# Optimization experiments

Measured on AMD Instinct MI355X. Metric: run time of the kernel, lower is better.

Reference implementation:

```python
import jax, jax.numpy as jnp
import numpy as np

DIM = 4096
N_HEADS = 32
N_KV_HEADS = 8
HEAD_DIM = DIM // N_HEADS  # 128
N_REP = N_HEADS // N_KV_HEADS  # 4
HIDDEN = 14336  # 4*dim -> 2/3 -> *1.3 -> round up to multiple of 256
EPS = 1e-6
BSZ, SEQLEN, CACHE_LEN = 1, 2048, 4096
ROPE_THETA = 500000.0


def setup_inputs() -> dict:
    key = jax.random.key(0)
    ks = jax.random.split(key, 16)
    s = 0.02
    x = jax.random.normal(ks[0], (BSZ, SEQLEN, DIM), jnp.float32)
    cache_k = jax.random.normal(ks[1], (BSZ, CACHE_LEN, N_KV_HEADS, HEAD_DIM), jnp.float32)
    cache_v = jax.random.normal(ks[2], (BSZ, CACHE_LEN, N_KV_HEADS, HEAD_DIM), jnp.float32)
    # causal mask over rolling cache: query i may attend to cache slot j <= (CACHE_LEN - SEQLEN) + i
    qi = jnp.arange(SEQLEN)[:, None]
    kj = jnp.arange(CACHE_LEN)[None, :]
    mask = jnp.where(kj <= (CACHE_LEN - SEQLEN) + qi, 0.0, -1e9).astype(jnp.float32)[None, None]
    # rotary freqs (cos/sin pairs) for the new seqlen positions (start of window here)
    inv = 1.0 / (ROPE_THETA ** (jnp.arange(0, HEAD_DIM, 2, dtype=jnp.float32) / HEAD_DIM))
    t = jnp.arange(SEQLEN, dtype=jnp.float32)
    ang = t[:, None] * inv[None, :]  # [S, HEAD_DIM//2]
    freqs_cis = jnp.stack([jnp.cos(ang), jnp.sin(ang)], axis=-1)  # [S, HD//2, 2]
    # params (stored as (in, out))
    wq = jax.random.normal(ks[3], (DIM, N_HEADS * HEAD_DIM), jnp.float32) * s
    wk = jax.random.normal(ks[4], (DIM, N_KV_HEADS * HEAD_DIM), jnp.float32) * s
    wv = jax.random.normal(ks[5], (DIM, N_KV_HEADS * HEAD_DIM), jnp.float32) * s
    wo = jax.random.normal(ks[6], (N_HEADS * HEAD_DIM, DIM), jnp.float32) * s
    w1 = jax.random.normal(ks[7], (DIM, HIDDEN), jnp.float32) * s
    w2 = jax.random.normal(ks[8], (HIDDEN, DIM), jnp.float32) * s
    w3 = jax.random.normal(ks[9], (DIM, HIDDEN), jnp.float32) * s
    attn_norm_w = jnp.ones((DIM,), jnp.float32)
    ffn_norm_w = jnp.ones((DIM,), jnp.float32)
    return dict(x=x, mask=mask, freqs_cis=freqs_cis, cache_k=cache_k, cache_v=cache_v,
                wq=wq, wk=wk, wv=wv, wo=wo, w1=w1, w2=w2, w3=w3,
                attn_norm_w=attn_norm_w, ffn_norm_w=ffn_norm_w)


def rmsnorm(x, w, eps=EPS):
    return x * jax.lax.rsqrt(jnp.mean(x * x, axis=-1, keepdims=True) + eps) * w


def apply_rope(xq, xk, freqs_cis):
    # xq: [B,S,Hq,D], xk: [B,S,Hkv,D]; freqs_cis: [S, D//2, 2]
    cos = freqs_cis[None, :, None, :, 0]  # [1,S,1,D//2]
    sin = freqs_cis[None, :, None, :, 1]
    def rot(t):
        tp = t.reshape(*t.shape[:-1], -1, 2)
        t0, t1 = tp[..., 0], tp[..., 1]
        o0 = t0 * cos - t1 * sin
        o1 = t0 * sin + t1 * cos
        return jnp.stack([o0, o1], axis=-1).reshape(t.shape)
    return rot(xq), rot(xk)


def reference(x, mask, freqs_cis, cache_k, cache_v, wq, wk, wv, wo, w1, w2, w3, attn_norm_w, ffn_norm_w):
    bsz, seqlen, _ = x.shape
    # --- attention norm ---
    xn = rmsnorm(x, attn_norm_w)
    # --- qkv ---
    xq = (xn @ wq).reshape(bsz, seqlen, N_HEADS, HEAD_DIM)
    xk = (xn @ wk).reshape(bsz, seqlen, N_KV_HEADS, HEAD_DIM)
    xv = (xn @ wv).reshape(bsz, seqlen, N_KV_HEADS, HEAD_DIM)
    xq, xk = apply_rope(xq, xk, freqs_cis)
    # --- rolling KV cache ---
    cache_k = jnp.concatenate([cache_k[:, seqlen:], xk], axis=1)  # [B,CL,Hkv,D]
    cache_v = jnp.concatenate([cache_v[:, seqlen:], xv], axis=1)
    keys = jnp.repeat(cache_k[:bsz], N_REP, axis=2)    # [B,CL,Hq,D]
    values = jnp.repeat(cache_v[:bsz], N_REP, axis=2)
    # --- attention ---
    scores = jnp.einsum('bqhd,bkhd->bhqk', xq, keys) / jnp.sqrt(jnp.float32(HEAD_DIM))
    scores = jax.nn.softmax(scores + mask, axis=-1)
    attn = jnp.einsum('bhqk,bkhd->bqhd', scores, values).reshape(bsz, seqlen, -1)
    h = x + attn @ wo
    # --- ffn (SwiGLU) ---
    hn = rmsnorm(h, ffn_norm_w)
    out = h + (jax.nn.silu(hn @ w1) * (hn @ w3)) @ w2
    return (out, cache_k, cache_v)
```

## Files before the change

kernel.cpp:

```cpp
#include <hip/hip_runtime.h>

typedef _Float16 h16;
typedef _Float16 h16x4 __attribute__((ext_vector_type(4)));
typedef _Float16 h16x8 __attribute__((ext_vector_type(8)));
typedef __fp16 fp16x2 __attribute__((ext_vector_type(2)));
typedef float f32x4 __attribute__((ext_vector_type(4)));
typedef float f32x16 __attribute__((ext_vector_type(16)));
typedef unsigned short u16;
typedef unsigned int u32;
typedef unsigned int u32x4 __attribute__((ext_vector_type(4)));

__device__ __forceinline__ f32x4 mfma16(h16x8 a, h16x8 b, f32x4 c) {
  return __builtin_amdgcn_mfma_f32_16x16x32_f16(a, b, c, 0, 0, 0);
}
__device__ __forceinline__ f32x16 mfma32(h16x8 a, h16x8 b, f32x16 c) {
  return __builtin_amdgcn_mfma_f32_32x32x16_f16(a, b, c, 0, 0, 0);
}
__device__ __forceinline__ float fexp2(float x) {
#if __has_builtin(__builtin_amdgcn_exp2f)
  return __builtin_amdgcn_exp2f(x);
#else
  return exp2f(x);
#endif
}
__device__ __forceinline__ u32 pkh(float a, float b) {
  fp16x2 t = __builtin_amdgcn_cvt_pkrtz(a, b);
  return __builtin_bit_cast(u32, t);
}

typedef const __attribute__((address_space(1))) void* gas_p;
typedef __attribute__((address_space(3))) void* las_p;
__device__ __forceinline__ void ldscp16(const void* g, void* l) {
  __builtin_amdgcn_global_load_lds((gas_p)g, (las_p)l, 16, 0, 0);
}
#define VMCNT(n) asm volatile("s_waitcnt vmcnt(" #n ")" ::: "memory")
#define SBAR() asm volatile("s_barrier" ::: "memory")

__global__ __launch_bounds__(256) void rmsnorm_k(
    const float* __restrict__ x, const float* __restrict__ w, h16* __restrict__ out) {
  const int row = blockIdx.x, t = threadIdx.x;
  const float* xr = x + (size_t)row * 4096;
  float4 v[4];
  float ss = 0.f;
#pragma unroll
  for (int j = 0; j < 4; j++) {
    v[j] = *(const float4*)(xr + 4 * t + 1024 * j);
    ss += v[j].x * v[j].x + v[j].y * v[j].y + v[j].z * v[j].z + v[j].w * v[j].w;
  }
#pragma unroll
  for (int off = 1; off < 64; off <<= 1) ss += __shfl_xor(ss, off, 64);
  __shared__ float red[4];
  if ((t & 63) == 0) red[t >> 6] = ss;
  __syncthreads();
  float scale = rsqrtf((red[0] + red[1] + red[2] + red[3]) * (1.f / 4096.f) + 1e-6f);
  h16* orow = out + (size_t)row * 4096;
#pragma unroll
  for (int j = 0; j < 4; j++) {
    float4 wv = *(const float4*)(w + 4 * t + 1024 * j);
    h16x4 o;
    o[0] = (h16)(v[j].x * scale * wv.x);
    o[1] = (h16)(v[j].y * scale * wv.y);
    o[2] = (h16)(v[j].z * scale * wv.z);
    o[3] = (h16)(v[j].w * scale * wv.w);
    *(h16x4*)(orow + 4 * t + 1024 * j) = o;
  }
}

__global__ __launch_bounds__(256) void convw_k(
    const float* __restrict__ W, h16* __restrict__ out, int rowN, int ktiles) {
  __shared__ u16 timg[8192];
  const int t = threadIdx.x, b = blockIdx.x, kt = blockIdx.y;
  const float* src = W + (size_t)(kt * 64) * rowN + b * 128;
#pragma unroll
  for (int i = 0; i < 8; i++) {
    int c = t + (i << 8);
    int krow = c >> 5, nc = (c & 31) << 2;
    float4 v = *(const float4*)(src + (size_t)krow * rowN + nc);
    int kc = krow >> 3, e = krow & 7;
    float vals[4] = {v.x, v.y, v.z, v.w};
#pragma unroll
    for (int j = 0; j < 4; j++) {
      int m = nc + j;
      h16 hv = (h16)vals[j];
      timg[(m << 6) + ((kc ^ (m & 7)) << 3) + e] = __builtin_bit_cast(u16, hv);
    }
  }
  __syncthreads();
  uint4* dst = (uint4*)(out + ((size_t)(b * ktiles + kt) << 13));
  const uint4* s4 = (const uint4*)timg;
#pragma unroll
  for (int i = 0; i < 4; i++) dst[t + (i << 8)] = s4[t + (i << 8)];
}

template <int EPI>
__global__ __launch_bounds__(512, 2) void gemm_k(
    const h16* __restrict__ A, const h16* __restrict__ Wt,
    float* outF, h16* outH, const float* resid, const h16* uin,
    int K, int lda, int ldo, int no0) {
  __shared__ u16 lds[3][24576];
  const int tid = threadIdx.x, lane = tid & 63;
  const int wv = tid >> 6, wr = wv >> 2, wc = wv & 3;
  const int g = lane >> 4, lr = lane & 15;
  const int m0 = blockIdx.y << 7, n0 = blockIdx.x << 8;
  const int ktiles = K >> 6;

  f32x4 acc[4][4];
#pragma unroll
  for (int i = 0; i < 4; i++)
#pragma unroll
    for (int j = 0; j < 4; j++) acc[i][j] = {0.f, 0.f, 0.f, 0.f};

  const int rA = tid >> 3;
  const int kcA = (tid & 7) ^ (rA & 7);
  const h16* gA = A + (size_t)(m0 + rA) * lda + (kcA << 3);
  const h16* gA2 = gA + (size_t)64 * lda;
  const h16* gB0 = Wt + (((size_t)(2 * blockIdx.x) * ktiles) << 13) + tid * 8;
  const h16* gB1 = Wt + (((size_t)(2 * blockIdx.x + 1) * ktiles) << 13) + tid * 8;

  auto issueA = [&](int t) {
    char* base = (char*)lds[t % 3];
    ldscp16(gA + t * 64, base + tid * 16);
    ldscp16(gA2 + t * 64, base + tid * 16 + 8192);
    ldscp16(gB0 + ((size_t)t << 13), base + 16384 + tid * 16);
    ldscp16(gB0 + ((size_t)t << 13) + 4096, base + 16384 + tid * 16 + 8192);
  };
  auto issueB = [&](int t) {
    char* base = (char*)lds[t % 3];
    ldscp16(gB1 + ((size_t)t << 13), base + 32768 + tid * 16);
    ldscp16(gB1 + ((size_t)t << 13) + 4096, base + 32768 + tid * 16 + 8192);
  };

  issueA(0); issueB(0); issueA(1); issueB(1);
  VMCNT(6);
  SBAR();

  for (int t = 0; t < ktiles; ++t) {
    const char* bp = (const char*)lds[t % 3];
    const bool more = (t + 2 < ktiles);
#pragma unroll
    for (int ks = 0; ks < 2; ++ks) {
      h16x8 av[4], bv[4];
      const int cc = (ks << 2) + g;
#pragma unroll
      for (int f = 0; f < 4; f++) {
        int row = (wr << 6) + (f << 4) + lr;
        av[f] = *(const h16x8*)(bp + row * 128 + ((cc ^ (row & 7)) << 4));
        int nr = (wc << 6) + (f << 4) + lr;
        bv[f] = *(const h16x8*)(bp + 16384 + nr * 128 + ((cc ^ (nr & 7)) << 4));
      }
      if (more) {
        if (ks == 0) issueA(t + 2);
        else issueB(t + 2);
      }
      __builtin_amdgcn_s_setprio(1);
#pragma unroll
      for (int fi = 0; fi < 4; fi++)
#pragma unroll
        for (int fj = 0; fj < 4; fj++)
          acc[fi][fj] = mfma16(av[fi], bv[fj], acc[fi][fj]);
      __builtin_amdgcn_s_setprio(0);
    }
    if (t + 1 < ktiles) {
      if (more) VMCNT(6);
      else VMCNT(0);
      SBAR();
    }
  }
#pragma unroll
  for (int fi = 0; fi < 4; fi++) {
    const int row = m0 + (wr << 6) + (fi << 4) + (g << 2);
#pragma unroll
    for (int fj = 0; fj < 4; fj++) {
      const int col = no0 + n0 + (wc << 6) + (fj << 4) + lr;
#pragma unroll
      for (int r = 0; r < 4; r++) {
        float vl = acc[fi][fj][r];
        if constexpr (EPI == 5) {
          if (col < 4096) outH[(size_t)(row + r) * 4096 + col] = (h16)vl;
          else outF[(size_t)(row + r) * 2048 + (col - 4096)] = vl;
        } else {
          size_t idx = (size_t)(row + r) * ldo + col;
          if constexpr (EPI == 1) outH[idx] = (h16)vl;
          else if constexpr (EPI == 2) outF[idx] = resid[idx] + vl;
          else if constexpr (EPI == 3) {
            float u = (float)uin[idx];
            outH[idx] = (h16)((u / (1.f + __expf(-u))) * vl);
          } else outF[idx] = outF[idx] + vl;
        }
      }
    }
  }
}

__global__ __launch_bounds__(256) void rope_q_k(
    const h16* __restrict__ qin, const float* __restrict__ freqs, h16* qout) {
  const int row = blockIdx.x, t = threadIdx.x;
  const float SCL = 0.12751743647239037f;
#pragma unroll
  for (int it = 0; it < 8; ++it) {
    int pid = t + 256 * it;
    int head = pid >> 6, pp = pid & 63;
    size_t idx = (size_t)row * 4096 + head * 128 + 2 * pp;
    float x0 = (float)qin[idx], x1 = (float)qin[idx + 1];
    float cs = freqs[row * 128 + 2 * pp], sn = freqs[row * 128 + 2 * pp + 1];
    qout[idx] = (h16)((x0 * cs - x1 * sn) * SCL);
    qout[idx + 1] = (h16)((x0 * sn + x1 * cs) * SCL);
  }
}

__global__ __launch_bounds__(256) void cache_build_k(
    const float* __restrict__ oldK, const float* __restrict__ oldV,
    const float* __restrict__ kvraw, const float* __restrict__ freqs,
    float* __restrict__ outK, float* __restrict__ outV,
    h16* __restrict__ Kf, h16* __restrict__ Vt) {
  const int rt = blockIdx.x, kvh = blockIdx.y;
  const int r0 = rt * 64, tid = threadIdx.x;
  __shared__ u16 vtile[64][128];
#pragma unroll
  for (int it = 0; it < 16; ++it) {
    int s = tid + 256 * it;
    int rr = s >> 6, pp = s & 63;
    int r = r0 + rr;
    float k0, k1, v0, v1;
    if (r < 2048) {
      const float* kp = oldK + (size_t)(r + 2048) * 1024 + kvh * 128 + 2 * pp;
      k0 = kp[0]; k1 = kp[1];
      const float* vp = oldV + (size_t)(r + 2048) * 1024 + kvh * 128 + 2 * pp;
      v0 = vp[0]; v1 = vp[1];
    } else {
      int tpos = r - 2048;
      const float* kp = kvraw + (size_t)tpos * 2048 + kvh * 128 + 2 * pp;
      float x0 = kp[0], x1 = kp[1];
      float cs = freqs[tpos * 128 + 2 * pp], sn = freqs[tpos * 128 + 2 * pp + 1];
      k0 = x0 * cs - x1 * sn;
      k1 = x0 * sn + x1 * cs;
      const float* vp = kvraw + (size_t)tpos * 2048 + 1024 + kvh * 128 + 2 * pp;
      v0 = vp[0]; v1 = vp[1];
    }
    size_t oidx = (size_t)r * 1024 + kvh * 128 + 2 * pp;
    outK[oidx] = k0; outK[oidx + 1] = k1;
    outV[oidx] = v0; outV[oidx + 1] = v1;
    size_t kfi = (size_t)kvh * 524288 + (size_t)r * 128 + 2 * pp;
    Kf[kfi] = (h16)k0; Kf[kfi + 1] = (h16)k1;
    h16 h0 = (h16)v0, h1 = (h16)v1;
    vtile[rr][2 * pp] = __builtin_bit_cast(u16, h0);
    vtile[rr][2 * pp + 1] = __builtin_bit_cast(u16, h1);
  }
  __syncthreads();
#pragma unroll
  for (int it = 0; it < 4; ++it) {
    int c = tid + 256 * it;
    int d = c >> 3, rg = c & 7;
    u16 tmp[8];
#pragma unroll
    for (int u = 0; u < 8; u++) tmp[u] = vtile[rg * 8 + u][d];
    *(uint4*)((u16*)Vt + (size_t)kvh * 524288 + (size_t)d * 4096 + r0 + rg * 8) =
        *(uint4*)tmp;
  }
}

__global__ __launch_bounds__(256, 2) void attn_k(
    const h16* __restrict__ Q, const h16* __restrict__ Kf,
    const h16* __restrict__ Vt, h16* __restrict__ O) {
  __shared__ u16 skv[2][16384];
  const int qt = 15 - blockIdx.x, h = blockIdx.y;
  const int q0 = qt << 7, kvh = h >> 2;
  const int tid = threadIdx.x, w = tid >> 6, lane = tid & 63;
  const int lq = lane & 31, lh = lane >> 5;
  const h16* Kb = Kf + (size_t)kvh * 524288;
  const h16* Vb = Vt + (size_t)kvh * 524288;
  const int qg = q0 + w * 32 + lq;

  h16x8 qv[8];
  {
    const h16* qp = Q + (size_t)qg * 4096 + h * 128 + (lh << 3);
#pragma unroll
    for (int c = 0; c < 8; c++) qv[c] = *(const h16x8*)(qp + c * 16);
  }
  h16x8 hone;
#pragma unroll
  for (int i = 0; i < 8; i++) hone[i] = (h16)1.0f;
  f32x16 oa[4], ol2;
#pragma unroll
  for (int d = 0; d < 4; d++)
#pragma unroll
    for (int v = 0; v < 16; v++) oa[d][v] = 0.f;
#pragma unroll
  for (int v = 0; v < 16; v++) ol2[v] = 0.f;
  float m2 = -3e38f;
  const int ntiles = 34 + 2 * qt;

  const int jK = tid >> 4, kch = tid & 15;
  const h16* gK = Kb + (size_t)jK * 128 + ((kch ^ (jK & 15)) << 3);
  const int dV = tid >> 3, jch = tid & 7;
  const h16* gV = Vb + (size_t)dV * 4096 + ((jch ^ (dV & 7)) << 3);

  auto issueK = [&](int jt) {
    char* base = (char*)skv[jt & 1];
    const h16* s = gK + (size_t)(jt << 6) * 128;
#pragma unroll
    for (int i = 0; i < 4; i++)
      ldscp16(s + (size_t)i * 2048, base + tid * 16 + i * 4096);
  };
  auto issueV = [&](int jt) {
    char* base = (char*)skv[jt & 1] + 16384;
    const h16* s = gV + (jt << 6);
#pragma unroll
    for (int i = 0; i < 4; i++)
      ldscp16(s + (size_t)i * 131072, base + tid * 16 + i * 4096);
  };

  issueK(0); issueV(0);
  VMCNT(0);
  SBAR();

  for (int jt = 0; jt < ntiles; ++jt) {
    const char* bp = (const char*)skv[jt & 1];
    const bool more = (jt + 1 < ntiles);
    if (more) issueK(jt + 1);
    f32x16 st[2];
#pragma unroll
    for (int jb = 0; jb < 2; jb++) {
      f32x16 s;
#pragma unroll
      for (int v = 0; v < 16; v++) s[v] = 0.f;
      const int jr = jb * 32 + lq;
      __builtin_amdgcn_s_setprio(1);
#pragma unroll
      for (int kc = 0; kc < 8; kc++) {
        h16x8 ak =
            *(const h16x8*)(bp + jr * 256 + ((((kc << 1) + lh) ^ (jr & 15)) << 4));
        s = mfma32(ak, qv[kc], s);
      }
      __builtin_amdgcn_s_setprio(0);
      st[jb] = s;
    }
    if (more) issueV(jt + 1);
    if (jt >= ntiles - 2) {
      const int j0 = jt << 6;
#pragma unroll
      for (int jb = 0; jb < 2; jb++)
#pragma unroll
        for (int v = 0; v < 16; v++) {
          int j = j0 + jb * 32 + (v & 3) + (((v >> 2) & 3) << 3) + (lh << 2);
          if (j > 2048 + qg) st[jb][v] = -1e30f;
        }
    }
    float pm = fmaxf(st[0][0], st[0][1]);
#pragma unroll
    for (int v = 2; v < 16; v += 2) pm = fmaxf(fmaxf(st[0][v], st[0][v + 1]), pm);
#pragma unroll
    for (int v = 0; v < 16; v += 2) pm = fmaxf(fmaxf(st[1][v], st[1][v + 1]), pm);
    pm = fmaxf(pm, __shfl_xor(pm, 32, 64));
    if (__any(pm - m2 > 8.f)) {
      float mn = fmaxf(m2, pm);
      float al = fexp2(m2 - mn);
      m2 = mn;
#pragma unroll
      for (int d = 0; d < 4; d++) oa[d] *= al;
      ol2 *= al;
    }
    u32 pw[2][8];
#pragma unroll
    for (int jb = 0; jb < 2; jb++)
#pragma unroll
      for (int c = 0; c < 4; c++) {
        float p0 = fexp2(st[jb][4 * c] - m2);
        float p1 = fexp2(st[jb][4 * c + 1] - m2);
        float p2 = fexp2(st[jb][4 * c + 2] - m2);
        float p3 = fexp2(st[jb][4 * c + 3] - m2);
        pw[jb][2 * c] = pkh(p0, p1);
        pw[jb][2 * c + 1] = pkh(p2, p3);
      }
    h16x8 pb[4];
#pragma unroll
    for (int kc = 0; kc < 4; kc++) {
      const int jb = kc >> 1, cb = (kc & 1) << 1;
      u32 oa_ = pw[jb][2 * cb], ob_ = pw[jb][2 * cb + 1];
      u32 oc_ = pw[jb][2 * cb + 2], od_ = pw[jb][2 * cb + 3];
      u32 s0 = lh ? oa_ : oc_, s1 = lh ? ob_ : od_;
      u32 r0 = __shfl_xor(s0, 32, 64), r1 = __shfl_xor(s1, 32, 64);
      u32x4 wds = {lh ? r0 : oa_, lh ? r1 : ob_, lh ? oc_ : r0, lh ? od_ : r1};
      pb[kc] = __builtin_bit_cast(h16x8, wds);
    }
    if (more) { VMCNT(8); } else { VMCNT(0); }
    __builtin_amdgcn_s_setprio(1);
#pragma unroll
    for (int d = 0; d < 4; d++) {
      const int dr = (d << 5) + lq;
#pragma unroll
      for (int kc = 0; kc < 4; kc++) {
        h16x8 av = *(const h16x8*)(bp + 16384 + dr * 128 +
                                   ((((kc << 1) + lh) ^ (dr & 7)) << 4));
        oa[d] = mfma32(av, pb[kc], oa[d]);
      }
    }
#pragma unroll
    for (int kc = 0; kc < 4; kc++) ol2 = mfma32(hone, pb[kc], ol2);
    __builtin_amdgcn_s_setprio(0);
    if (more) {
      VMCNT(4);
      SBAR();
    }
  }
  float rl = 1.f / ol2[0];
  h16* Op = O + (size_t)qg * 4096 + h * 128;
#pragma unroll
  for (int d = 0; d < 4; d++)
#pragma unroll
    for (int b = 0; b < 4; b++) {
      h16x4 ov;
#pragma unroll
      for (int i = 0; i < 4; i++) ov[i] = (h16)(oa[d][(b << 2) + i] * rl);
      *(h16x4*)(Op + (d << 5) + (b << 3) + (lh << 2)) = ov;
    }
}

extern "C" void kernel_launch(void* const* d_in, const int* in_sizes, int n_in,
                              void* d_out, int out_size, void* d_ws, size_t ws_size,
                              hipStream_t stream) {
  const float* x = (const float*)d_in[0];
  const float* freqs = (const float*)d_in[2];
  const float* oldK = (const float*)d_in[3];
  const float* oldV = (const float*)d_in[4];
  const float* wq = (const float*)d_in[5];
  const float* wk = (const float*)d_in[6];
  const float* wvp = (const float*)d_in[7];
  const float* wo = (const float*)d_in[8];
  const float* w1 = (const float*)d_in[9];
  const float* w2 = (const float*)d_in[10];
  const float* w3 = (const float*)d_in[11];
  const float* anw = (const float*)d_in[12];
  const float* fnw = (const float*)d_in[13];
  float* out = (float*)d_out;
  float* outK = out + 8388608;
  float* outV = out + 12582912;

  char* ws = (char*)d_ws;
  h16* xn = (h16*)(ws + 0);
  h16* bufW = (h16*)(ws + 16777216);
  float* hbuf = (float*)(ws + 75497472);
  float* kvraw = (float*)(ws + 75497472);
  h16* kf = (h16*)(ws + 92274688);
  h16* vt = (h16*)(ws + 100663296);
  h16* ub = (h16*)(ws + 109051904);
  h16* qraw = (h16*)(ws + 109051904);
  h16* attnb = (h16*)(ws + 125829120);

  rmsnorm_k<<<2048, 256, 0, stream>>>(x, anw, xn);
  convw_k<<<dim3(32, 64), 256, 0, stream>>>(wq, bufW, 4096, 64);
  convw_k<<<dim3(8, 64), 256, 0, stream>>>(wk, bufW + ((size_t)32 * 64 << 13), 1024, 64);
  convw_k<<<dim3(8, 64), 256, 0, stream>>>(wvp, bufW + ((size_t)40 * 64 << 13), 1024, 64);
  gemm_k<5><<<dim3(24, 16), 512, 0, stream>>>(xn, bufW, kvraw, qraw, nullptr,
                                              nullptr, 4096, 4096, 0, 0);
  rope_q_k<<<2048, 256, 0, stream>>>(qraw, freqs, qraw);
  cache_build_k<<<dim3(64, 8), 256, 0, stream>>>(oldK, oldV, kvraw, freqs, outK,
                                                 outV, kf, vt);
  attn_k<<<dim3(16, 32), 256, 0, stream>>>(qraw, kf, vt, attnb);
  convw_k<<<dim3(32, 64), 256, 0, stream>>>(wo, bufW, 4096, 64);
  gemm_k<2><<<dim3(16, 16), 512, 0, stream>>>(attnb, bufW, hbuf, nullptr, x,
                                              nullptr, 4096, 4096, 4096, 0);
  rmsnorm_k<<<2048, 256, 0, stream>>>(hbuf, fnw, xn);
  convw_k<<<dim3(56, 64), 256, 0, stream>>>(w1, bufW, 14336, 64);
  gemm_k<1><<<dim3(28, 16), 512, 0, stream>>>(xn, bufW, nullptr, ub, nullptr,
                                              nullptr, 4096, 4096, 14336, 0);
  convw_k<<<dim3(56, 64), 256, 0, stream>>>(w1 + 7168, bufW, 14336, 64);
  gemm_k<1><<<dim3(28, 16), 512, 0, stream>>>(xn, bufW, nullptr, ub, nullptr,
                                              nullptr, 4096, 4096, 14336, 7168);
  convw_k<<<dim3(56, 64), 256, 0, stream>>>(w3, bufW, 14336, 64);
  gemm_k<3><<<dim3(28, 16), 512, 0, stream>>>(xn, bufW, nullptr, ub, nullptr, ub,
                                              4096, 4096, 14336, 0);
  convw_k<<<dim3(56, 64), 256, 0, stream>>>(w3 + 7168, bufW, 14336, 64);
  gemm_k<3><<<dim3(28, 16), 512, 0, stream>>>(xn, bufW, nullptr, ub, nullptr, ub,
                                              4096, 4096, 14336, 7168);
  convw_k<<<dim3(32, 112), 256, 0, stream>>>(w2, bufW, 4096, 112);
  gemm_k<2><<<dim3(16, 16), 512, 0, stream>>>(ub, bufW, out, nullptr, hbuf,
                                              nullptr, 7168, 14336, 4096, 0);
  convw_k<<<dim3(32, 112), 256, 0, stream>>>(w2 + (size_t)7168 * 4096, bufW, 4096, 112);
  gemm_k<4><<<dim3(16, 16), 512, 0, stream>>>(ub + 7168, bufW, out, nullptr,
                                              nullptr, nullptr, 7168, 14336, 4096, 0);
}
```

Baseline: 1.526 ms.

## Load GEMM A operand directly from global into registers, stage only B in LDS

The GEMM no longer stages the activation (A) tile in shared memory. Each wave loads its A fragments straight from global memory into double-buffered registers, while only the weight tiles go through the triple-buffered LDS pipeline. This shrinks LDS per block, removes the LDS reads and bank traffic for A, and the main loop is unrolled by two to alternate the register buffers. The costs are higher register pressure (launch bounds dropped to 1 block per SM), loss of A reuse across the four column waves (each wave reloads its A rows from global/L2), and new manual vmcnt accounting that must stay correct.

```diff
diff --git a/kernel.cpp b/kernel.cpp
--- a/kernel.cpp
+++ b/kernel.cpp
@@ -93,11 +93,11 @@
 }
 
 template <int EPI>
-__global__ __launch_bounds__(512, 2) void gemm_k(
+__global__ __launch_bounds__(512, 1) void gemm_k(
     const h16* __restrict__ A, const h16* __restrict__ Wt,
     float* outF, h16* outH, const float* resid, const h16* uin,
     int K, int lda, int ldo, int no0) {
-  __shared__ u16 lds[3][24576];
+  __shared__ u16 lds[3][16384];
   const int tid = threadIdx.x, lane = tid & 63;
   const int wv = tid >> 6, wr = wv >> 2, wc = wv & 3;
   const int g = lane >> 4, lr = lane & 15;
@@ -110,60 +110,86 @@
 #pragma unroll
     for (int j = 0; j < 4; j++) acc[i][j] = {0.f, 0.f, 0.f, 0.f};
 
-  const int rA = tid >> 3;
-  const int kcA = (tid & 7) ^ (rA & 7);
-  const h16* gA = A + (size_t)(m0 + rA) * lda + (kcA << 3);
-  const h16* gA2 = gA + (size_t)64 * lda;
   const h16* gB0 = Wt + (((size_t)(2 * blockIdx.x) * ktiles) << 13) + tid * 8;
   const h16* gB1 = Wt + (((size_t)(2 * blockIdx.x + 1) * ktiles) << 13) + tid * 8;
-
-  auto issueA = [&](int t) {
-    char* base = (char*)lds[t % 3];
-    ldscp16(gA + t * 64, base + tid * 16);
-    ldscp16(gA2 + t * 64, base + tid * 16 + 8192);
-    ldscp16(gB0 + ((size_t)t << 13), base + 16384 + tid * 16);
-    ldscp16(gB0 + ((size_t)t << 13) + 4096, base + 16384 + tid * 16 + 8192);
-  };
+  const h16* gAf = A + (size_t)(m0 + (wr << 6) + lr) * lda + (g << 3);
+  const size_t fstride = (size_t)16 * lda;
+
   auto issueB = [&](int t) {
     char* base = (char*)lds[t % 3];
-    ldscp16(gB1 + ((size_t)t << 13), base + 32768 + tid * 16);
-    ldscp16(gB1 + ((size_t)t << 13) + 4096, base + 32768 + tid * 16 + 8192);
+    ldscp16(gB0 + ((size_t)t << 13), base + tid * 16);
+    ldscp16(gB0 + ((size_t)t << 13) + 4096, base + tid * 16 + 8192);
+    ldscp16(gB1 + ((size_t)t << 13), base + 16384 + tid * 16);
+    ldscp16(gB1 + ((size_t)t << 13) + 4096, base + 16384 + tid * 16 + 8192);
   };
-
-  issueA(0); issueB(0); issueA(1); issueB(1);
-  VMCNT(6);
-  SBAR();
-
-  for (int t = 0; t < ktiles; ++t) {
-    const char* bp = (const char*)lds[t % 3];
-    const bool more = (t + 2 < ktiles);
-#pragma unroll
-    for (int ks = 0; ks < 2; ++ks) {
-      h16x8 av[4], bv[4];
-      const int cc = (ks << 2) + g;
-#pragma unroll
-      for (int f = 0; f < 4; f++) {
-        int row = (wr << 6) + (f << 4) + lr;
-        av[f] = *(const h16x8*)(bp + row * 128 + ((cc ^ (row & 7)) << 4));
-        int nr = (wc << 6) + (f << 4) + lr;
-        bv[f] = *(const h16x8*)(bp + 16384 + nr * 128 + ((cc ^ (nr & 7)) << 4));
-      }
-      if (more) {
-        if (ks == 0) issueA(t + 2);
-        else issueB(t + 2);
-      }
-      __builtin_amdgcn_s_setprio(1);
-#pragma unroll
-      for (int fi = 0; fi < 4; fi++)
-#pragma unroll
-        for (int fj = 0; fj < 4; fj++)
-          acc[fi][fj] = mfma16(av[fi], bv[fj], acc[fi][fj]);
-      __builtin_amdgcn_s_setprio(0);
-    }
-    if (t + 1 < ktiles) {
-      if (more) VMCNT(6);
-      else VMCNT(0);
+  h16x8 avA[2][4], avB[2][4];
+  auto loadA = [&](h16x8(&dst)[2][4], int t) {
+    const h16* p = gAf + t * 64;
+#pragma unroll
+    for (int ks = 0; ks < 2; ks++)
+#pragma unroll
+      for (int f = 0; f < 4; f++)
+        dst[ks][f] = *(const h16x8*)(p + f * fstride + ks * 32);
+  };
+
+  issueB(0);
+  loadA(avA, 0);
+  issueB(1);
+  loadA(avB, 1);
+
+  for (int t = 0; t < ktiles; t += 2) {
+    {
+      if (t + 1 < ktiles) { VMCNT(20); } else { VMCNT(8); }
       SBAR();
+      const char* bp = (const char*)lds[t % 3];
+#pragma unroll
+      for (int ks = 0; ks < 2; ++ks) {
+        h16x8 bv[4];
+        const int cc = (ks << 2) + g;
+#pragma unroll
+        for (int f = 0; f < 4; f++) {
+          int nr = (wc << 6) + (f << 4) + lr;
+          bv[f] = *(const h16x8*)(bp + nr * 128 + ((cc ^ (nr & 7)) << 4));
+        }
+        __builtin_amdgcn_s_setprio(1);
+#pragma unroll
+        for (int fi = 0; fi < 4; fi++)
+#pragma unroll
+          for (int fj = 0; fj < 4; fj++)
+            acc[fi][fj] = mfma16(avA[ks][fi], bv[fj], acc[fi][fj]);
+        __builtin_amdgcn_s_setprio(0);
+      }
+      if (t + 2 < ktiles) {
+        issueB(t + 2);
+        loadA(avA, t + 2);
+      }
+    }
+    {
+      const int t1 = t + 1;
+      if (t1 + 1 < ktiles) { VMCNT(20); } else { VMCNT(8); }
+      SBAR();
+      const char* bp = (const char*)lds[t1 % 3];
+#pragma unroll
+      for (int ks = 0; ks < 2; ++ks) {
+        h16x8 bv[4];
+        const int cc = (ks << 2) + g;
+#pragma unroll
+        for (int f = 0; f < 4; f++) {
+          int nr = (wc << 6) + (f << 4) + lr;
+          bv[f] = *(const h16x8*)(bp + nr * 128 + ((cc ^ (nr & 7)) << 4));
+        }
+        __builtin_amdgcn_s_setprio(1);
+#pragma unroll
+        for (int fi = 0; fi < 4; fi++)
+#pragma unroll
+          for (int fj = 0; fj < 4; fj++)
+            acc[fi][fj] = mfma16(avB[ks][fi], bv[fj], acc[fi][fj]);
+        __builtin_amdgcn_s_setprio(0);
+      }
+      if (t1 + 2 < ktiles) {
+        issueB(t1 + 2);
+        loadA(avB, t1 + 2);
+      }
     }
   }
 #pragma unroll
```

New measurement: 2.494 ms. 63.4% more time.

## Shrink GEMM tile to 128x128 with 256 threads and double buffering

Applied to the files above, without the earlier changes.

The GEMM kernel changes from a 128x256 tile with 8 waves and a 3-stage LDS pipeline to a 128x128 tile with 4 waves and 2 LDS buffers. Loads for tile t+2 are now issued after a barrier at the end of each iteration rather than interleaved with the MFMA steps. All launches double their grid x dimension to match. The aim is more blocks and lower LDS use per block for better occupancy. In exchange it reloads A more often, lowers arithmetic intensity and adds a second barrier per k-step that exposes load latency.

```diff
diff --git a/kernel.cpp b/kernel.cpp
--- a/kernel.cpp
+++ b/kernel.cpp
@@ -93,15 +93,15 @@
 }
 
 template <int EPI>
-__global__ __launch_bounds__(512, 2) void gemm_k(
+__global__ __launch_bounds__(256, 2) void gemm_k(
     const h16* __restrict__ A, const h16* __restrict__ Wt,
     float* outF, h16* outH, const float* resid, const h16* uin,
     int K, int lda, int ldo, int no0) {
-  __shared__ u16 lds[3][24576];
+  __shared__ u16 lds[2][16384];
   const int tid = threadIdx.x, lane = tid & 63;
-  const int wv = tid >> 6, wr = wv >> 2, wc = wv & 3;
+  const int wv = tid >> 6, wr = wv >> 1, wc = wv & 1;
   const int g = lane >> 4, lr = lane & 15;
-  const int m0 = blockIdx.y << 7, n0 = blockIdx.x << 8;
+  const int m0 = blockIdx.y << 7, n0 = blockIdx.x << 7;
   const int ktiles = K >> 6;
 
   f32x4 acc[4][4];
@@ -110,33 +110,30 @@
 #pragma unroll
     for (int j = 0; j < 4; j++) acc[i][j] = {0.f, 0.f, 0.f, 0.f};
 
-  const int rA = tid >> 3;
-  const int kcA = (tid & 7) ^ (rA & 7);
-  const h16* gA = A + (size_t)(m0 + rA) * lda + (kcA << 3);
-  const h16* gA2 = gA + (size_t)64 * lda;
-  const h16* gB0 = Wt + (((size_t)(2 * blockIdx.x) * ktiles) << 13) + tid * 8;
-  const h16* gB1 = Wt + (((size_t)(2 * blockIdx.x + 1) * ktiles) << 13) + tid * 8;
-
-  auto issueA = [&](int t) {
-    char* base = (char*)lds[t % 3];
-    ldscp16(gA + t * 64, base + tid * 16);
-    ldscp16(gA2 + t * 64, base + tid * 16 + 8192);
-    ldscp16(gB0 + ((size_t)t << 13), base + 16384 + tid * 16);
-    ldscp16(gB0 + ((size_t)t << 13) + 4096, base + 16384 + tid * 16 + 8192);
+  const int rA = tid >> 1;
+  const int kcA = ((tid & 1) << 2);
+  const h16* gB = Wt + (((size_t)blockIdx.x * ktiles) << 13) + tid * 8;
+
+  auto issue = [&](int t) {
+    char* base = (char*)lds[t & 1];
+#pragma unroll
+    for (int i = 0; i < 4; i++) {
+      int c = tid + (i << 8);
+      int r = c >> 3, ch = (c & 7) ^ ((c >> 3) & 7);
+      ldscp16(A + (size_t)(m0 + r) * lda + t * 64 + (ch << 3), base + c * 16);
+    }
+#pragma unroll
+    for (int i = 0; i < 4; i++)
+      ldscp16(gB + ((size_t)t << 13) + (i << 11), base + 16384 + tid * 16 + (i << 12));
   };
-  auto issueB = [&](int t) {
-    char* base = (char*)lds[t % 3];
-    ldscp16(gB1 + ((size_t)t << 13), base + 32768 + tid * 16);
-    ldscp16(gB1 + ((size_t)t << 13) + 4096, base + 32768 + tid * 16 + 8192);
-  };
-
-  issueA(0); issueB(0); issueA(1); issueB(1);
-  VMCNT(6);
-  SBAR();
+
+  issue(0);
+  issue(1);
 
   for (int t = 0; t < ktiles; ++t) {
-    const char* bp = (const char*)lds[t % 3];
-    const bool more = (t + 2 < ktiles);
+    if (t + 1 < ktiles) { VMCNT(8); } else { VMCNT(0); }
+    SBAR();
+    const char* bp = (const char*)lds[t & 1];
 #pragma unroll
     for (int ks = 0; ks < 2; ++ks) {
       h16x8 av[4], bv[4];
@@ -148,10 +145,6 @@
         int nr = (wc << 6) + (f << 4) + lr;
         bv[f] = *(const h16x8*)(bp + 16384 + nr * 128 + ((cc ^ (nr & 7)) << 4));
       }
-      if (more) {
-        if (ks == 0) issueA(t + 2);
-        else issueB(t + 2);
-      }
       __builtin_amdgcn_s_setprio(1);
 #pragma unroll
       for (int fi = 0; fi < 4; fi++)
@@ -160,11 +153,8 @@
           acc[fi][fj] = mfma16(av[fi], bv[fj], acc[fi][fj]);
       __builtin_amdgcn_s_setprio(0);
     }
-    if (t + 1 < ktiles) {
-      if (more) VMCNT(6);
-      else VMCNT(0);
-      SBAR();
-    }
+    SBAR();
+    if (t + 2 < ktiles) issue(t + 2);
   }
 #pragma unroll
   for (int fi = 0; fi < 4; fi++) {
@@ -451,32 +441,32 @@
   convw_k<<<dim3(32, 64), 256, 0, stream>>>(wq, bufW, 4096, 64);
   convw_k<<<dim3(8, 64), 256, 0, stream>>>(wk, bufW + ((size_t)32 * 64 << 13), 1024, 64);
   convw_k<<<dim3(8, 64), 256, 0, stream>>>(wvp, bufW + ((size_t)40 * 64 << 13), 1024, 64);
-  gemm_k<5><<<dim3(24, 16), 512, 0, stream>>>(xn, bufW, kvraw, qraw, nullptr,
+  gemm_k<5><<<dim3(48, 16), 256, 0, stream>>>(xn, bufW, kvraw, qraw, nullptr,
                                               nullptr, 4096, 4096, 0, 0);
   rope_q_k<<<2048, 256, 0, stream>>>(qraw, freqs, qraw);
   cache_build_k<<<dim3(64, 8), 256, 0, stream>>>(oldK, oldV, kvraw, freqs, outK,
                                                  outV, kf, vt);
   attn_k<<<dim3(16, 32), 256, 0, stream>>>(qraw, kf, vt, attnb);
   convw_k<<<dim3(32, 64), 256, 0, stream>>>(wo, bufW, 4096, 64);
-  gemm_k<2><<<dim3(16, 16), 512, 0, stream>>>(attnb, bufW, hbuf, nullptr, x,
+  gemm_k<2><<<dim3(32, 16), 256, 0, stream>>>(attnb, bufW, hbuf, nullptr, x,
                                               nullptr, 4096, 4096, 4096, 0);
   rmsnorm_k<<<2048, 256, 0, stream>>>(hbuf, fnw, xn);
   convw_k<<<dim3(56, 64), 256, 0, stream>>>(w1, bufW, 14336, 64);
-  gemm_k<1><<<dim3(28, 16), 512, 0, stream>>>(xn, bufW, nullptr, ub, nullptr,
+  gemm_k<1><<<dim3(56, 16), 256, 0, stream>>>(xn, bufW, nullptr, ub, nullptr,
                                               nullptr, 4096, 4096, 14336, 0);
   convw_k<<<dim3(56, 64), 256, 0, stream>>>(w1 + 7168, bufW, 14336, 64);
-  gemm_k<1><<<dim3(28, 16), 512, 0, stream>>>(xn, bufW, nullptr, ub, nullptr,
+  gemm_k<1><<<dim3(56, 16), 256, 0, stream>>>(xn, bufW, nullptr, ub, nullptr,
                                               nullptr, 4096, 4096, 14336, 7168);
   convw_k<<<dim3(56, 64), 256, 0, stream>>>(w3, bufW, 14336, 64);
-  gemm_k<3><<<dim3(28, 16), 512, 0, stream>>>(xn, bufW, nullptr, ub, nullptr, ub,
+  gemm_k<3><<<dim3(56, 16), 256, 0, stream>>>(xn, bufW, nullptr, ub, nullptr, ub,
                                               4096, 4096, 14336, 0);
   convw_k<<<dim3(56, 64), 256, 0, stream>>>(w3 + 7168, bufW, 14336, 64);
-  gemm_k<3><<<dim3(28, 16), 512, 0, stream>>>(xn, bufW, nullptr, ub, nullptr, ub,
+  gemm_k<3><<<dim3(56, 16), 256, 0, stream>>>(xn, bufW, nullptr, ub, nullptr, ub,
                                               4096, 4096, 14336, 7168);
   convw_k<<<dim3(32, 112), 256, 0, stream>>>(w2, bufW, 4096, 112);
-  gemm_k<2><<<dim3(16, 16), 512, 0, stream>>>(ub, bufW, out, nullptr, hbuf,
+  gemm_k<2><<<dim3(32, 16), 256, 0, stream>>>(ub, bufW, out, nullptr, hbuf,
                                               nullptr, 7168, 14336, 4096, 0);
   convw_k<<<dim3(32, 112), 256, 0, stream>>>(w2 + (size_t)7168 * 4096, bufW, 4096, 112);
-  gemm_k<4><<<dim3(16, 16), 512, 0, stream>>>(ub + 7168, bufW, out, nullptr,
+  gemm_k<4><<<dim3(32, 16), 256, 0, stream>>>(ub + 7168, bufW, out, nullptr,
                                               nullptr, nullptr, 7168, 14336, 4096, 0);
 }
```

New measurement: 1.527 ms. Within noise of the previous version (+0.1%).
